# Kernel tuning notes

Measured on AMD Instinct MI355X. Metric: run time of the kernel, lower is better.

The kernel has to match this reference:

```python
import jax, jax.numpy as jnp
import numpy as np

EMBED_DIM = 1024
HEADS = 16
DIM_HEAD = 64  # embed_dim // heads
SCALE = DIM_HEAD ** -0.5


def setup_inputs() -> dict:
    key = jax.random.key(0)
    ks = jax.random.split(key, 6)
    x = jax.random.normal(ks[0], (2, 2048, EMBED_DIM), dtype=jnp.float32)
    # qkv_proj: Linear(embed_dim, 3*embed_dim) with bias
    w_qkv = jax.random.normal(ks[1], (EMBED_DIM, 3 * EMBED_DIM), dtype=jnp.float32) * (EMBED_DIM ** -0.5)
    b_qkv = jax.random.normal(ks[2], (3 * EMBED_DIM,), dtype=jnp.float32) * 0.01
    # out_proj: Linear(embed_dim, embed_dim) with bias
    w_out = jax.random.normal(ks[3], (EMBED_DIM, EMBED_DIM), dtype=jnp.float32) * (EMBED_DIM ** -0.5)
    b_out = jax.random.normal(ks[4], (EMBED_DIM,), dtype=jnp.float32) * 0.01
    return {"x": x, "w_qkv": w_qkv, "b_qkv": b_qkv, "w_out": w_out, "b_out": b_out}


def reference(x, w_qkv, b_qkv, w_out, b_out):
    b, s, d = x.shape
    h, dh = HEADS, d // HEADS
    qkv = x @ w_qkv + b_qkv                       # [b, s, 3d]
    qkv = qkv.reshape(b, s, 3, h, dh)
    qkv = jnp.transpose(qkv, (0, 3, 2, 1, 4))     # [b, h, 3, s, dh]
    q, k, v = qkv[:, :, 0], qkv[:, :, 1], qkv[:, :, 2]
    q = q * SCALE
    attn = jnp.einsum("bhqd,bhkd->bhqk", q, k)    # [b, h, s, s]
    attn = jax.nn.softmax(attn.astype(jnp.float32), axis=-1).astype(attn.dtype)
    # attn_dropout p=0 -> identity
    out = jnp.einsum("bhqk,bhkd->bhqd", attn, v)  # [b, h, s, dh]
    out = jnp.transpose(out, (0, 2, 1, 3)).reshape(b, s, d)
    return out @ w_out + b_out
```

## Files before the change

### kernel.cpp

```cpp
#include <hip/hip_runtime.h>

#define EMBED  1024
#define HEADS  16
#define DHEAD  64
#define SEQ    2048
#define BATCH  2
#define NTOK   4096
#define QS2    (0.125f * 1.44269504089f)
#define DEFER_THR 8.0f

typedef unsigned short u16t;
typedef float f32x4 __attribute__((ext_vector_type(4)));
typedef __bf16 bf16x8 __attribute__((ext_vector_type(8)));
typedef u16t u16x8 __attribute__((ext_vector_type(8)));
typedef u16t u16x4 __attribute__((ext_vector_type(4)));
typedef unsigned u32x4 __attribute__((ext_vector_type(4)));

static __device__ __forceinline__ u16t f2bf(float f) {
    unsigned u = __builtin_bit_cast(unsigned, f);
    return (u16t)((u + 0x7fffu + ((u >> 16) & 1u)) >> 16);
}
static __device__ __forceinline__ bf16x8 asbf(u16x8 v) {
    return __builtin_bit_cast(bf16x8, v);
}
static __device__ __forceinline__ f32x4 mfma16(bf16x8 a, bf16x8 b, f32x4 c) {
    return __builtin_amdgcn_mfma_f32_16x16x32_bf16(a, b, c, 0, 0, 0);
}
static __device__ __forceinline__ unsigned cvtpk(float lo, float hi) {
    unsigned r;
    asm("v_cvt_pk_bf16_f32 %0, %1, %2" : "=v"(r) : "v"(lo), "v"(hi));
    return r;
}

typedef const __attribute__((address_space(1))) void* as1cv;
typedef __attribute__((address_space(3))) void* as3v;
static __device__ __forceinline__ void ldsload16(const void* g, void* l) {
    __builtin_amdgcn_global_load_lds((as1cv)g, (as3v)l, 16, 0, 0);
}

__global__ __launch_bounds__(256)
void xcvt(const float* __restrict__ X, u16t* __restrict__ XB)
{
    const size_t i = ((size_t)blockIdx.x * 256 + threadIdx.x) * 8;
    float4 a = *(const float4*)&X[i];
    float4 b = *(const float4*)&X[i + 4];
    u16x8 o;
    o[0] = f2bf(a.x); o[1] = f2bf(a.y); o[2] = f2bf(a.z); o[3] = f2bf(a.w);
    o[4] = f2bf(b.x); o[5] = f2bf(b.y); o[6] = f2bf(b.z); o[7] = f2bf(b.w);
    *(u16x8*)&XB[i] = o;
}

__global__ __launch_bounds__(256)
void wtrans(const float* __restrict__ W, u16t* __restrict__ WT, int K, int N)
{
    __shared__ float L[64][65];
    const int t = threadIdx.x;
    const int k0 = blockIdx.y * 64, n0 = blockIdx.x * 64;
#pragma unroll
    for (int rep = 0; rep < 4; ++rep) {
        const int id = rep * 256 + t;
        const int kk = id >> 4, nc = (id & 15) * 4;
        float4 v = *(const float4*)&W[(size_t)(k0 + kk) * N + n0 + nc];
        L[kk][nc] = v.x; L[kk][nc + 1] = v.y; L[kk][nc + 2] = v.z; L[kk][nc + 3] = v.w;
    }
    __syncthreads();
#pragma unroll
    for (int rep = 0; rep < 2; ++rep) {
        const int id = rep * 256 + t;
        const int n = id >> 3, kc = (id & 7) * 8;
        u16x8 o;
#pragma unroll
        for (int i = 0; i < 8; ++i) o[i] = f2bf(L[kc + i][n]);
        *(u16x8*)&WT[(size_t)(n0 + n) * K + k0 + kc] = o;
    }
}

__global__ __launch_bounds__(256)
void vtrans(const u16t* __restrict__ V, u16t* __restrict__ Vt)
{
    __shared__ u16t L[64][65];
    const int t = threadIdx.x;
    const int bh = blockIdx.y;
    const int s0 = blockIdx.x * 64;
    const u16t* src = V + ((size_t)bh * SEQ + s0) * DHEAD;
#pragma unroll
    for (int rep = 0; rep < 2; ++rep) {
        const int id = rep * 256 + t;
        const int s = id >> 3, dc = (id & 7) * 8;
        u16x8 v = *(const u16x8*)&src[(size_t)s * DHEAD + dc];
#pragma unroll
        for (int i = 0; i < 8; ++i) L[s][dc + i] = v[i];
    }
    __syncthreads();
    u16t* dstb = Vt + (size_t)bh * DHEAD * SEQ + s0;
#pragma unroll
    for (int rep = 0; rep < 2; ++rep) {
        const int id = rep * 256 + t;
        const int d = id >> 3, sc = (id & 7) * 8;
        u16x8 o;
#pragma unroll
        for (int i = 0; i < 8; ++i) o[i] = L[sc + i][d];
        *(u16x8*)&dstb[(size_t)d * SEQ + sc] = o;
    }
}

__global__ __launch_bounds__(256)
void gemm_bf16(const u16t* __restrict__ A, const u16t* __restrict__ BT,
               const float* __restrict__ bias, int N, int mode,
               float* __restrict__ C0, u16t* __restrict__ Qo,
               u16t* __restrict__ Ko, u16t* __restrict__ Vo)
{
    __shared__ __align__(16) u16t Al[128 * 64];
    __shared__ __align__(16) u16t Bl[128 * 64];
    const int t = threadIdx.x;
    const int lane = t & 63;
    const int g = lane >> 4, l15 = lane & 15;
    const int w = t >> 6, wr = w >> 1, wc = w & 1;
    const int m0 = blockIdx.y * 128, n0 = blockIdx.x * 128;

    const int srow = w * 32;
    const int lrow = lane >> 3;
    const int lcol = (lane & 7) * 8;

    f32x4 acc[4][4] = {};

    for (int k0 = 0; k0 < EMBED; k0 += 64) {
        __syncthreads();
#pragma unroll
        for (int r = 0; r < 4; ++r) {
            const int row = srow + r * 8;
            ldsload16(&A [(size_t)(m0 + row + lrow) * EMBED + k0 + lcol], &Al[row * 64]);
            ldsload16(&BT[(size_t)(n0 + row + lrow) * EMBED + k0 + lcol], &Bl[row * 64]);
        }
        __syncthreads();
#pragma unroll
        for (int kk = 0; kk < 2; ++kk) {
            bf16x8 av[4], bv[4];
#pragma unroll
            for (int i = 0; i < 4; ++i) {
                av[i] = asbf(*(const u16x8*)&Al[(wr * 64 + i * 16 + l15) * 64 + kk * 32 + g * 8]);
                bv[i] = asbf(*(const u16x8*)&Bl[(wc * 64 + i * 16 + l15) * 64 + kk * 32 + g * 8]);
            }
#pragma unroll
            for (int i = 0; i < 4; ++i)
#pragma unroll
                for (int j = 0; j < 4; ++j)
                    acc[i][j] = mfma16(av[i], bv[j], acc[i][j]);
        }
    }

#pragma unroll
    for (int i = 0; i < 4; ++i)
#pragma unroll
        for (int j = 0; j < 4; ++j)
#pragma unroll
            for (int r = 0; r < 4; ++r) {
                const int row = m0 + wr * 64 + i * 16 + g * 4 + r;
                const int col = n0 + wc * 64 + j * 16 + l15;
                float v = acc[i][j][r] + bias[col];
                if (mode == 0) {
                    C0[(size_t)row * N + col] = v;
                } else {
                    const int tt = col >> 10, c1 = col & 1023;
                    const int h = c1 >> 6, d = c1 & 63;
                    const int b = row >> 11, s = row & 2047;
                    if (tt == 0) v *= QS2;
                    u16t* dst = (tt == 0) ? Qo : (tt == 1 ? Ko : Vo);
                    dst[(((size_t)b * HEADS + h) * SEQ + s) * DHEAD + d] = f2bf(v);
                }
            }
}

__global__ __launch_bounds__(256)
void attn_mfma(const u16t* __restrict__ Q, const u16t* __restrict__ K,
               const u16t* __restrict__ Vt, u16t* __restrict__ AO)
{
    __shared__ __align__(16) u16t Kl[64][72];
    __shared__ __align__(16) u16t Vl[64][72];
    const int t = threadIdx.x;
    const int lane = t & 63, wq = t >> 6;
    const int g = lane >> 4, l15 = lane & 15;
    const int bh = blockIdx.y;
    const int q0 = blockIdx.x * 64;
    const int b = bh >> 4, h = bh & 15;

    const u16t* qrow = Q + ((size_t)bh * SEQ + q0 + wq * 16 + l15) * DHEAD;
    bf16x8 qf[2];
    qf[0] = asbf(*(const u16x8*)&qrow[g * 8]);
    qf[1] = asbf(*(const u16x8*)&qrow[32 + g * 8]);

    const int srow = t >> 3, scol = (t & 7) * 8;
    const u16t* Kb = K + (size_t)bh * SEQ * DHEAD;
    const u16t* Vb = Vt + (size_t)bh * DHEAD * SEQ;

    f32x4 accO[4] = {};
    float mrun = -1e30f, lrun = 0.f;

    for (int kv0 = 0; kv0 < SEQ; kv0 += 64) {
        __syncthreads();
#pragma unroll
        for (int rep = 0; rep < 2; ++rep) {
            const int r = rep * 32 + srow;
            *(u16x8*)&Kl[r][scol] = *(const u16x8*)&Kb[(size_t)(kv0 + r) * DHEAD + scol];
            *(u16x8*)&Vl[r][scol] = *(const u16x8*)&Vb[(size_t)r * SEQ + kv0 + scol];
        }
        __syncthreads();

        f32x4 s4[4] = {};
#pragma unroll
        for (int kk = 0; kk < 2; ++kk)
#pragma unroll
            for (int mf = 0; mf < 4; ++mf) {
                bf16x8 a = asbf(*(const u16x8*)&Kl[mf * 16 + l15][kk * 32 + g * 8]);
                s4[mf] = mfma16(a, qf[kk], s4[mf]);
            }

        float mt = s4[0][0];
#pragma unroll
        for (int mf = 0; mf < 4; ++mf)
#pragma unroll
            for (int r = 0; r < 4; ++r) mt = fmaxf(mt, s4[mf][r]);
        mt = fmaxf(mt, __shfl_xor(mt, 16));
        mt = fmaxf(mt, __shfl_xor(mt, 32));

        const bool skip = __all(mt - mrun <= DEFER_THR) != 0;
        const float mnew = skip ? mrun : fmaxf(mrun, mt);

        float p[4][4]; float rs = 0.f;
#pragma unroll
        for (int mf = 0; mf < 4; ++mf)
#pragma unroll
            for (int r = 0; r < 4; ++r) {
                p[mf][r] = __builtin_amdgcn_exp2f(s4[mf][r] - mnew);
                rs += p[mf][r];
            }
        rs += __shfl_xor(rs, 16);
        rs += __shfl_xor(rs, 32);

        if (skip) {
            lrun += rs;
        } else {
            const float alpha = __builtin_amdgcn_exp2f(mrun - mnew);
            lrun = lrun * alpha + rs;
            mrun = mnew;
            float al[4];
#pragma unroll
            for (int r = 0; r < 4; ++r) al[r] = __shfl(alpha, g * 4 + r);
#pragma unroll
            for (int nf = 0; nf < 4; ++nf)
#pragma unroll
                for (int r = 0; r < 4; ++r) accO[nf][r] *= al[r];
        }

        u16x8 pu[2];
#pragma unroll
        for (int kk = 0; kk < 2; ++kk) {
            const int a = kk * 2;
            u32x4 pw;
            pw[0] = cvtpk(p[a][0], p[a][1]);
            pw[1] = cvtpk(p[a][2], p[a][3]);
            pw[2] = cvtpk(p[a + 1][0], p[a + 1][1]);
            pw[3] = cvtpk(p[a + 1][2], p[a + 1][3]);
            pu[kk] = __builtin_bit_cast(u16x8, pw);
        }

#pragma unroll
        for (int kk = 0; kk < 2; ++kk)
#pragma unroll
            for (int nf = 0; nf < 4; ++nf) {
                const u16t* vr = &Vl[nf * 16 + l15][0];
                u16x4 lo = *(const u16x4*)&vr[kk * 32 + g * 4];
                u16x4 hi = *(const u16x4*)&vr[kk * 32 + 16 + g * 4];
                u16x8 bb = __builtin_shufflevector(lo, hi, 0, 1, 2, 3, 4, 5, 6, 7);
                accO[nf] = mfma16(asbf(pu[kk]), asbf(bb), accO[nf]);
            }
    }

    const float inv = 1.f / lrun;
    float iv[4];
#pragma unroll
    for (int r = 0; r < 4; ++r) iv[r] = __shfl(inv, g * 4 + r);
#pragma unroll
    for (int nf = 0; nf < 4; ++nf)
#pragma unroll
        for (int r = 0; r < 4; ++r) {
            const int s = q0 + wq * 16 + g * 4 + r;
            AO[((size_t)b * SEQ + s) * EMBED + h * DHEAD + nf * 16 + l15] =
                f2bf(accO[nf][r] * iv[r]);
        }
}

extern "C" void kernel_launch(void* const* d_in, const int* in_sizes, int n_in,
                              void* d_out, int out_size, void* d_ws, size_t ws_size,
                              hipStream_t stream)
{
    const float* x     = (const float*)d_in[0];
    const float* w_qkv = (const float*)d_in[1];
    const float* b_qkv = (const float*)d_in[2];
    const float* w_out = (const float*)d_in[3];
    const float* b_out = (const float*)d_in[4];

    u16t* xb  = (u16t*)d_ws;
    u16t* wqt = xb  + (size_t)NTOK * EMBED;
    u16t* wot = wqt + (size_t)3072 * 1024;
    u16t* Qb  = wot + (size_t)1024 * 1024;
    u16t* Kb  = Qb  + (size_t)NTOK * EMBED;
    u16t* Vb  = Kb  + (size_t)NTOK * EMBED;
    u16t* Vtb = Vb  + (size_t)NTOK * EMBED;
    u16t* AOb = Vtb + (size_t)NTOK * EMBED;

    xcvt<<<2048, 256, 0, stream>>>(x, xb);
    wtrans<<<dim3(48, 16), 256, 0, stream>>>(w_qkv, wqt, 1024, 3072);
    wtrans<<<dim3(16, 16), 256, 0, stream>>>(w_out, wot, 1024, 1024);

    gemm_bf16<<<dim3(24, 32), 256, 0, stream>>>(xb, wqt, b_qkv, 3072, 1,
                                                nullptr, Qb, Kb, Vb);
    vtrans<<<dim3(32, 32), 256, 0, stream>>>(Vb, Vtb);
    attn_mfma<<<dim3(32, 32), 256, 0, stream>>>(Qb, Kb, Vtb, AOb);
    gemm_bf16<<<dim3(8, 32), 256, 0, stream>>>(AOb, wot, b_out, 1024, 0,
                                               (float*)d_out, nullptr, nullptr, nullptr);
}
```

Baseline: 242.8 us.

## Double-buffer GEMM LDS tiles and prefetch K/V while doubling attention query tile

The GEMM now uses two LDS buffers so the next k-tile's async load is issued before computing the current one, dropping one barrier per iteration. The attention kernel processes 128 queries per block (32 per wave, two MFMA query halves), which reuses each K/V LDS tile for twice the queries. It also prefetches the next K/V tile into registers during compute. The costs are doubled GEMM LDS use, more registers in attention, and half as many attention blocks (512), which may reduce occupancy.

Result: no change. 241.7 us (-0.4%).

```diff
diff --git a/kernel.cpp b/kernel.cpp
--- a/kernel.cpp
+++ b/kernel.cpp
@@ -110,8 +110,8 @@
                float* __restrict__ C0, u16t* __restrict__ Qo,
                u16t* __restrict__ Ko, u16t* __restrict__ Vo)
 {
-    __shared__ __align__(16) u16t Al[128 * 64];
-    __shared__ __align__(16) u16t Bl[128 * 64];
+    __shared__ __align__(16) u16t Al[2][128 * 64];
+    __shared__ __align__(16) u16t Bl[2][128 * 64];
     const int t = threadIdx.x;
     const int lane = t & 63;
     const int g = lane >> 4, l15 = lane & 15;
@@ -122,24 +122,35 @@
     const int lrow = lane >> 3;
     const int lcol = (lane & 7) * 8;
 
+#define GSTAGE(buf, k0)                                                          \
+    {                                                                            \
+        _Pragma("unroll")                                                        \
+        for (int r_ = 0; r_ < 4; ++r_) {                                         \
+            const int row_ = srow + r_ * 8;                                      \
+            ldsload16(&A [(size_t)(m0 + row_ + lrow) * EMBED + (k0) + lcol],     \
+                      &Al[buf][row_ * 64]);                                      \
+            ldsload16(&BT[(size_t)(n0 + row_ + lrow) * EMBED + (k0) + lcol],     \
+                      &Bl[buf][row_ * 64]);                                      \
+        }                                                                        \
+    }
+
     f32x4 acc[4][4] = {};
 
+    GSTAGE(0, 0);
+    __syncthreads();
+
+    int cur = 0;
     for (int k0 = 0; k0 < EMBED; k0 += 64) {
-        __syncthreads();
-#pragma unroll
-        for (int r = 0; r < 4; ++r) {
-            const int row = srow + r * 8;
-            ldsload16(&A [(size_t)(m0 + row + lrow) * EMBED + k0 + lcol], &Al[row * 64]);
-            ldsload16(&BT[(size_t)(n0 + row + lrow) * EMBED + k0 + lcol], &Bl[row * 64]);
-        }
-        __syncthreads();
+        if (k0 + 64 < EMBED) GSTAGE(cur ^ 1, k0 + 64);
+        const u16t* Ab = &Al[cur][0];
+        const u16t* Bb = &Bl[cur][0];
 #pragma unroll
         for (int kk = 0; kk < 2; ++kk) {
             bf16x8 av[4], bv[4];
 #pragma unroll
             for (int i = 0; i < 4; ++i) {
-                av[i] = asbf(*(const u16x8*)&Al[(wr * 64 + i * 16 + l15) * 64 + kk * 32 + g * 8]);
-                bv[i] = asbf(*(const u16x8*)&Bl[(wc * 64 + i * 16 + l15) * 64 + kk * 32 + g * 8]);
+                av[i] = asbf(*(const u16x8*)&Ab[(wr * 64 + i * 16 + l15) * 64 + kk * 32 + g * 8]);
+                bv[i] = asbf(*(const u16x8*)&Bb[(wc * 64 + i * 16 + l15) * 64 + kk * 32 + g * 8]);
             }
 #pragma unroll
             for (int i = 0; i < 4; ++i)
@@ -147,7 +158,10 @@
                 for (int j = 0; j < 4; ++j)
                     acc[i][j] = mfma16(av[i], bv[j], acc[i][j]);
         }
-    }
+        __syncthreads();
+        cur ^= 1;
+    }
+#undef GSTAGE
 
 #pragma unroll
     for (int i = 0; i < 4; ++i)
@@ -181,88 +195,130 @@
     const int lane = t & 63, wq = t >> 6;
     const int g = lane >> 4, l15 = lane & 15;
     const int bh = blockIdx.y;
-    const int q0 = blockIdx.x * 64;
+    const int q0 = blockIdx.x * 128;
     const int b = bh >> 4, h = bh & 15;
 
-    const u16t* qrow = Q + ((size_t)bh * SEQ + q0 + wq * 16 + l15) * DHEAD;
-    bf16x8 qf[2];
-    qf[0] = asbf(*(const u16x8*)&qrow[g * 8]);
-    qf[1] = asbf(*(const u16x8*)&qrow[32 + g * 8]);
+    const u16t* qbase = Q + ((size_t)bh * SEQ + q0 + wq * 32) * DHEAD;
+    bf16x8 qf[2][2];
+#pragma unroll
+    for (int qh = 0; qh < 2; ++qh)
+#pragma unroll
+        for (int kk = 0; kk < 2; ++kk)
+            qf[qh][kk] = asbf(*(const u16x8*)&qbase[(size_t)(qh * 16 + l15) * DHEAD + kk * 32 + g * 8]);
 
     const int srow = t >> 3, scol = (t & 7) * 8;
     const u16t* Kb = K + (size_t)bh * SEQ * DHEAD;
     const u16t* Vb = Vt + (size_t)bh * DHEAD * SEQ;
 
-    f32x4 accO[4] = {};
-    float mrun = -1e30f, lrun = 0.f;
-
-    for (int kv0 = 0; kv0 < SEQ; kv0 += 64) {
-        __syncthreads();
+    {
+        u16x8 k0r[2], v0r[2];
 #pragma unroll
         for (int rep = 0; rep < 2; ++rep) {
             const int r = rep * 32 + srow;
-            *(u16x8*)&Kl[r][scol] = *(const u16x8*)&Kb[(size_t)(kv0 + r) * DHEAD + scol];
-            *(u16x8*)&Vl[r][scol] = *(const u16x8*)&Vb[(size_t)r * SEQ + kv0 + scol];
-        }
-        __syncthreads();
-
-        f32x4 s4[4] = {};
+            k0r[rep] = *(const u16x8*)&Kb[(size_t)r * DHEAD + scol];
+            v0r[rep] = *(const u16x8*)&Vb[(size_t)r * SEQ + scol];
+        }
+#pragma unroll
+        for (int rep = 0; rep < 2; ++rep) {
+            const int r = rep * 32 + srow;
+            *(u16x8*)&Kl[r][scol] = k0r[rep];
+            *(u16x8*)&Vl[r][scol] = v0r[rep];
+        }
+    }
+    __syncthreads();
+
+    f32x4 accO[4][2] = {};
+    float mrun[2] = {-1e30f, -1e30f}, lrun[2] = {0.f, 0.f};
+
+    for (int kv0 = 0; kv0 < SEQ; kv0 += 64) {
+        const bool more = (kv0 + 64 < SEQ);
+        u16x8 kreg[2], vreg[2];
+        if (more) {
+#pragma unroll
+            for (int rep = 0; rep < 2; ++rep) {
+                const int r = rep * 32 + srow;
+                kreg[rep] = *(const u16x8*)&Kb[(size_t)(kv0 + 64 + r) * DHEAD + scol];
+                vreg[rep] = *(const u16x8*)&Vb[(size_t)r * SEQ + kv0 + 64 + scol];
+            }
+        }
+
+        f32x4 s4[4][2] = {};
 #pragma unroll
         for (int kk = 0; kk < 2; ++kk)
 #pragma unroll
             for (int mf = 0; mf < 4; ++mf) {
                 bf16x8 a = asbf(*(const u16x8*)&Kl[mf * 16 + l15][kk * 32 + g * 8]);
-                s4[mf] = mfma16(a, qf[kk], s4[mf]);
-            }
-
-        float mt = s4[0][0];
+                s4[mf][0] = mfma16(a, qf[0][kk], s4[mf][0]);
+                s4[mf][1] = mfma16(a, qf[1][kk], s4[mf][1]);
+            }
+
+        float mt[2];
+#pragma unroll
+        for (int qh = 0; qh < 2; ++qh) {
+            float m = s4[0][qh][0];
+#pragma unroll
+            for (int mf = 0; mf < 4; ++mf)
+#pragma unroll
+                for (int r = 0; r < 4; ++r) m = fmaxf(m, s4[mf][qh][r]);
+            m = fmaxf(m, __shfl_xor(m, 16));
+            m = fmaxf(m, __shfl_xor(m, 32));
+            mt[qh] = m;
+        }
+        const bool skip =
+            __all((mt[0] - mrun[0] <= DEFER_THR) && (mt[1] - mrun[1] <= DEFER_THR)) != 0;
+        float mnew[2];
+#pragma unroll
+        for (int qh = 0; qh < 2; ++qh)
+            mnew[qh] = skip ? mrun[qh] : fmaxf(mrun[qh], mt[qh]);
+
+        float p[4][2][4], rs[2] = {0.f, 0.f};
 #pragma unroll
         for (int mf = 0; mf < 4; ++mf)
 #pragma unroll
-            for (int r = 0; r < 4; ++r) mt = fmaxf(mt, s4[mf][r]);
-        mt = fmaxf(mt, __shfl_xor(mt, 16));
-        mt = fmaxf(mt, __shfl_xor(mt, 32));
-
-        const bool skip = __all(mt - mrun <= DEFER_THR) != 0;
-        const float mnew = skip ? mrun : fmaxf(mrun, mt);
-
-        float p[4][4]; float rs = 0.f;
-#pragma unroll
-        for (int mf = 0; mf < 4; ++mf)
-#pragma unroll
-            for (int r = 0; r < 4; ++r) {
-                p[mf][r] = __builtin_amdgcn_exp2f(s4[mf][r] - mnew);
-                rs += p[mf][r];
-            }
-        rs += __shfl_xor(rs, 16);
-        rs += __shfl_xor(rs, 32);
+            for (int qh = 0; qh < 2; ++qh)
+#pragma unroll
+                for (int r = 0; r < 4; ++r) {
+                    p[mf][qh][r] = __builtin_amdgcn_exp2f(s4[mf][qh][r] - mnew[qh]);
+                    rs[qh] += p[mf][qh][r];
+                }
+#pragma unroll
+        for (int qh = 0; qh < 2; ++qh) {
+            rs[qh] += __shfl_xor(rs[qh], 16);
+            rs[qh] += __shfl_xor(rs[qh], 32);
+        }
 
         if (skip) {
-            lrun += rs;
+            lrun[0] += rs[0];
+            lrun[1] += rs[1];
         } else {
-            const float alpha = __builtin_amdgcn_exp2f(mrun - mnew);
-            lrun = lrun * alpha + rs;
-            mrun = mnew;
-            float al[4];
-#pragma unroll
-            for (int r = 0; r < 4; ++r) al[r] = __shfl(alpha, g * 4 + r);
-#pragma unroll
-            for (int nf = 0; nf < 4; ++nf)
-#pragma unroll
-                for (int r = 0; r < 4; ++r) accO[nf][r] *= al[r];
-        }
-
-        u16x8 pu[2];
-#pragma unroll
-        for (int kk = 0; kk < 2; ++kk) {
-            const int a = kk * 2;
-            u32x4 pw;
-            pw[0] = cvtpk(p[a][0], p[a][1]);
-            pw[1] = cvtpk(p[a][2], p[a][3]);
-            pw[2] = cvtpk(p[a + 1][0], p[a + 1][1]);
-            pw[3] = cvtpk(p[a + 1][2], p[a + 1][3]);
-            pu[kk] = __builtin_bit_cast(u16x8, pw);
-        }
+#pragma unroll
+            for (int qh = 0; qh < 2; ++qh) {
+                const float alpha = __builtin_amdgcn_exp2f(mrun[qh] - mnew[qh]);
+                lrun[qh] = lrun[qh] * alpha + rs[qh];
+                mrun[qh] = mnew[qh];
+                float al[4];
+#pragma unroll
+                for (int r = 0; r < 4; ++r) al[r] = __shfl(alpha, g * 4 + r);
+#pragma unroll
+                for (int nf = 0; nf < 4; ++nf)
+#pragma unroll
+                    for (int r = 0; r < 4; ++r) accO[nf][qh][r] *= al[r];
+            }
+        }
+
+        u16x8 pu[2][2];
+#pragma unroll
+        for (int kk = 0; kk < 2; ++kk)
+#pragma unroll
+            for (int qh = 0; qh < 2; ++qh) {
+                const int a = kk * 2;
+                u32x4 pw;
+                pw[0] = cvtpk(p[a][qh][0], p[a][qh][1]);
+                pw[1] = cvtpk(p[a][qh][2], p[a][qh][3]);
+                pw[2] = cvtpk(p[a + 1][qh][0], p[a + 1][qh][1]);
+                pw[3] = cvtpk(p[a + 1][qh][2], p[a + 1][qh][3]);
+                pu[kk][qh] = __builtin_bit_cast(u16x8, pw);
+            }
 
 #pragma unroll
         for (int kk = 0; kk < 2; ++kk)
@@ -272,22 +328,37 @@
                 u16x4 lo = *(const u16x4*)&vr[kk * 32 + g * 4];
                 u16x4 hi = *(const u16x4*)&vr[kk * 32 + 16 + g * 4];
                 u16x8 bb = __builtin_shufflevector(lo, hi, 0, 1, 2, 3, 4, 5, 6, 7);
-                accO[nf] = mfma16(asbf(pu[kk]), asbf(bb), accO[nf]);
-            }
-    }
-
-    const float inv = 1.f / lrun;
-    float iv[4];
-#pragma unroll
-    for (int r = 0; r < 4; ++r) iv[r] = __shfl(inv, g * 4 + r);
-#pragma unroll
-    for (int nf = 0; nf < 4; ++nf)
-#pragma unroll
-        for (int r = 0; r < 4; ++r) {
-            const int s = q0 + wq * 16 + g * 4 + r;
-            AO[((size_t)b * SEQ + s) * EMBED + h * DHEAD + nf * 16 + l15] =
-                f2bf(accO[nf][r] * iv[r]);
-        }
+                accO[nf][0] = mfma16(asbf(pu[kk][0]), asbf(bb), accO[nf][0]);
+                accO[nf][1] = mfma16(asbf(pu[kk][1]), asbf(bb), accO[nf][1]);
+            }
+
+        __syncthreads();
+        if (more) {
+#pragma unroll
+            for (int rep = 0; rep < 2; ++rep) {
+                const int r = rep * 32 + srow;
+                *(u16x8*)&Kl[r][scol] = kreg[rep];
+                *(u16x8*)&Vl[r][scol] = vreg[rep];
+            }
+            __syncthreads();
+        }
+    }
+
+#pragma unroll
+    for (int qh = 0; qh < 2; ++qh) {
+        const float inv = 1.f / lrun[qh];
+        float iv[4];
+#pragma unroll
+        for (int r = 0; r < 4; ++r) iv[r] = __shfl(inv, g * 4 + r);
+#pragma unroll
+        for (int nf = 0; nf < 4; ++nf)
+#pragma unroll
+            for (int r = 0; r < 4; ++r) {
+                const int s = q0 + wq * 32 + qh * 16 + g * 4 + r;
+                AO[((size_t)b * SEQ + s) * EMBED + h * DHEAD + nf * 16 + l15] =
+                    f2bf(accO[nf][qh][r] * iv[r]);
+            }
+    }
 }
 
 extern "C" void kernel_launch(void* const* d_in, const int* in_sizes, int n_in,
@@ -316,7 +387,7 @@
     gemm_bf16<<<dim3(24, 32), 256, 0, stream>>>(xb, wqt, b_qkv, 3072, 1,
                                                 nullptr, Qb, Kb, Vb);
     vtrans<<<dim3(32, 32), 256, 0, stream>>>(Vb, Vtb);
-    attn_mfma<<<dim3(32, 32), 256, 0, stream>>>(Qb, Kb, Vtb, AOb);
+    attn_mfma<<<dim3(16, 32), 256, 0, stream>>>(Qb, Kb, Vtb, AOb);
     gemm_bf16<<<dim3(8, 32), 256, 0, stream>>>(AOb, wot, b_out, 1024, 0,
                                                (float*)d_out, nullptr, nullptr, nullptr);
 }
```
